# Performance work log

Hardware: AMD Instinct MI355X
Metric: run time of the kernel (lower is better)

## Reference

```python
import jax, jax.numpy as jnp
import numpy as np

G, K = 60, 13  # SO(3) group size, neighbors per group element


def _gather(x, nei):
    # x: [N, C, G] -> [N, C, G, K] via fixed neighbor indices (len G*K)
    return x[:, :, nei].reshape(x.shape[0], x.shape[1], G, K)


def _comb(x, nei, W, b):
    # gather-then-(1,K)-Conv2d == contraction over (channel, neighbor)
    d = _gather(x, nei)                                   # [N,C,G,K]
    return jnp.einsum('ncgk,ock->nog', d, W) + b[None, :, None]


def setup_inputs() -> dict:
    key = jax.random.key(0)
    ks = jax.random.split(key, 8)
    N = 512
    feats = jax.random.normal(ks[0], (N, 32, G), jnp.float32)
    nei = jax.random.randint(ks[1], (G * K,), 0, G, jnp.int32)

    def w(k, o, c):
        return jax.random.normal(k, (o, c, K), jnp.float32) * (1.0 / np.sqrt(c * K))

    return {
        'feats': feats, 'nei': nei,
        'W_in': w(ks[2], 256, 32), 'b_in': jnp.zeros((256,), jnp.float32),
        'W_r1': w(ks[3], 512, 256), 'b_r1': jnp.zeros((512,), jnp.float32),
        'W_r2': w(ks[4], 256, 512), 'b_r2': jnp.zeros((256,), jnp.float32),
        'W_out': w(ks[5], 32, 256), 'b_out': jnp.zeros((32,), jnp.float32),
    }


def reference(feats, nei, W_in, b_in, W_r1, b_r1, W_r2, b_r2, W_out, b_out):
    # Conv_in: gather + (1,13) conv, 32 -> 256
    h = _comb(feats, nei, W_in, b_in)                      # [N,256,G]
    # Residual_Comb_Conv(256, 512, 256)
    r = jax.nn.relu(_comb(h, nei, W_r1, b_r1))             # [N,512,G]
    h = h + _comb(r, nei, W_r2, b_r2)                      # [N,256,G]
    # Conv_out: gather + (1,13) conv, 256 -> 32, then outer residual
    feats_eqv = _comb(h, nei, W_out, b_out) + feats        # [N,32,G]
    feats_inv = jnp.mean(feats_eqv, axis=-1)               # [N,32]
    feats_eqv = feats_eqv / jnp.maximum(
        jnp.linalg.norm(feats_eqv, axis=1, keepdims=True), 1e-4)
    feats_inv = feats_inv / jnp.maximum(
        jnp.linalg.norm(feats_inv, axis=1, keepdims=True), 1e-4)
    return feats_inv, feats_eqv
```

## Files before the change

### kernel.cpp

```cpp
#include <hip/hip_runtime.h>
#include <stdint.h>

#define GSZ 60
#define KNB 13
#define NPT 512

typedef __attribute__((ext_vector_type(4))) float f32x4;
typedef __attribute__((ext_vector_type(8))) short s16x8;

__device__ __forceinline__ ushort f2bf(float f) {
  union { float f; unsigned u; } v; v.f = f;
  unsigned r = v.u + 0x7fffu + ((v.u >> 16) & 1u);
  return (ushort)(r >> 16);
}
__device__ __forceinline__ float bf2f(ushort h) {
  union { unsigned u; float f; } v; v.u = ((unsigned)h) << 16;
  return v.f;
}

__device__ __forceinline__ void gload_lds16(const void* gsrc, void* ldst) {
  __builtin_amdgcn_global_load_lds(
      (const __attribute__((address_space(1))) uint32_t*)gsrc,
      (__attribute__((address_space(3))) uint32_t*)ldst, 16, 0, 0);
}

__global__ __launch_bounds__(256) void prep_feats_k(const float* __restrict__ feats,
                                                    ushort* __restrict__ X0) {
  int idx = blockIdx.x * 256 + threadIdx.x;
  if (idx >= 61 * NPT * 32) return;
  int c = idx & 31;
  int t = idx >> 5;
  int n = t % NPT;
  int g = t / NPT;
  X0[idx] = (g < GSZ) ? f2bf(feats[(n * 32 + c) * GSZ + g]) : (ushort)0;
}

__global__ __launch_bounds__(256) void prep_wb_k(const float* __restrict__ W,
                                                 ushort* __restrict__ Wb,
                                                 int O, int OPAD, int C, int KPAD) {
  int idx = blockIdx.x * 256 + threadIdx.x;
  if (idx >= OPAD * KPAD) return;
  int o = idx / KPAD;
  int kk = idx - o * KPAD;
  int k = kk / C;
  int c = kk - k * C;
  Wb[idx] = (o < O && k < KNB) ? f2bf(W[(o * C + c) * KNB + k]) : (ushort)0;
}

template <int CIN, int KTOT, int OPAD, int OREAL, int BN, int MODE, bool RELU>
__global__ __launch_bounds__(256) void comb_gemm(
    const ushort* __restrict__ Xin,
    const ushort* __restrict__ Wb,
    const float* __restrict__ bias,
    const int* __restrict__ nei,
    ushort* __restrict__ Xout,
    float* __restrict__ Eq,
    const float* __restrict__ feats)
{
  constexpr int BM = 128;
  constexpr int BK = 64;
  constexpr int NCH = KTOT / BK;
  constexpr int TO = OPAD / BN;
  constexpr int TN = NPT / BM;
  constexpr int WN = BN / 2;
  constexpr int N_REP = WN / 16;
  constexpr int M_REP = 4;
  constexpr int CSH = (CIN == 32) ? 5 : (CIN == 256) ? 8 : 9;
  static_assert(CIN == (1 << CSH), "CIN pow2");

  __shared__ ushort smA[2][BM * BK];
  __shared__ ushort smB[2][BN * BK];
  __shared__ int nei_sh[16];

  const int nwg = TO * TN * GSZ;
  const int cpx = nwg >> 3;
  const int bid = blockIdx.x;
  const int idx = (bid & 7) * cpx + (bid >> 3);
  const int g = idx / (TO * TN);
  const int rem = idx - g * (TO * TN);
  const int nt = rem / TO;
  const int ot = rem - nt * TO;
  const int n0 = nt * BM;
  const int o0 = ot * BN;

  const int t = threadIdx.x;
  if (t < 14) nei_sh[t] = (t < KNB) ? nei[g * KNB + t] : GSZ;
  __syncthreads();

  const int w = t >> 6;
  const int l = t & 63;
  const int lrow = l & 15;
  const int lkg = l >> 4;
  const int wr = w >> 1;
  const int wc = w & 1;
  const int srow_w = w * 8;
  const int sr = l >> 3;
  const int slot = l & 7;

  int laneA[BM / 32], laneB[BN / 32], swz[BM / 32];
#pragma unroll
  for (int j = 0; j < BM / 32; ++j) {
    const int r = j * 32 + srow_w + sr;
    swz[j] = (slot ^ (r & 7)) << 3;
    laneA[j] = ((n0 + r) << CSH) + swz[j];
  }
#pragma unroll
  for (int j = 0; j < BN / 32; ++j) {
    const int r = j * 32 + srow_w + sr;
    laneB[j] = (o0 + r) * KTOT + ((slot ^ (r & 7)) << 3);
  }

  auto stage = [&](int buf, int q) {
    const int c0 = q * BK;
    if constexpr (CIN >= 64) {
      const int pbase = nei_sh[c0 >> CSH] * (NPT << CSH) + (c0 & (CIN - 1));
#pragma unroll
      for (int j = 0; j < BM / 32; ++j)
        gload_lds16(Xin + pbase + laneA[j], &smA[buf][(j * 32 + srow_w) * BK]);
    } else {
#pragma unroll
      for (int j = 0; j < BM / 32; ++j) {
        const int r = j * 32 + srow_w + sr;
        const int kk = c0 + swz[j];
        const int nbr = kk >> CSH;
        const int cc = kk & (CIN - 1);
        gload_lds16(Xin + ((nei_sh[nbr] * NPT + n0 + r) << CSH) + cc,
                    &smA[buf][(j * 32 + srow_w) * BK]);
      }
    }
#pragma unroll
    for (int j = 0; j < BN / 32; ++j)
      gload_lds16(Wb + laneB[j] + c0, &smB[buf][(j * 32 + srow_w) * BK]);
  };

  f32x4 acc[M_REP][N_REP] = {};

  stage(0, 0);
  asm volatile("s_waitcnt vmcnt(0)" ::: "memory");
  __builtin_amdgcn_s_barrier();

  int cur = 0;
#pragma unroll 1
  for (int q = 0; q < NCH; ++q) {
    if (q + 1 < NCH) stage(cur ^ 1, q + 1);
#pragma unroll
    for (int ks = 0; ks < 2; ++ks) {
      const int cb = ks * 4 + lkg;
      s16x8 bf[N_REP];
#pragma unroll
      for (int n = 0; n < N_REP; ++n) {
        const int r = wc * WN + n * 16 + lrow;
        bf[n] = *(const s16x8*)&smB[cur][r * BK + ((cb ^ (r & 7)) << 3)];
      }
#pragma unroll
      for (int m = 0; m < M_REP; ++m) {
        const int r = wr * 64 + m * 16 + lrow;
        s16x8 af = *(const s16x8*)&smA[cur][r * BK + ((cb ^ (r & 7)) << 3)];
#pragma unroll
        for (int n = 0; n < N_REP; ++n)
          acc[m][n] = __builtin_amdgcn_mfma_f32_16x16x32_bf16(af, bf[n], acc[m][n], 0, 0, 0);
      }
    }
    asm volatile("s_waitcnt vmcnt(0)" ::: "memory");
    __builtin_amdgcn_s_barrier();
    cur ^= 1;
  }

#pragma unroll
  for (int m = 0; m < M_REP; ++m) {
#pragma unroll
    for (int n = 0; n < N_REP; ++n) {
      const int oc = o0 + wc * WN + n * 16 + lrow;
      float bv;
      if (MODE == 2)
        bv = (oc < OREAL) ? bias[oc] : 0.f;
      else
        bv = bias[oc];
#pragma unroll
      for (int r = 0; r < 4; ++r) {
        const int row = n0 + wr * 64 + m * 16 + lkg * 4 + r;
        float v = acc[m][n][r] + bv;
        if (MODE == 0) {
          if (RELU) v = v > 0.f ? v : 0.f;
          Xout[((size_t)g * NPT + row) * OPAD + oc] = f2bf(v);
        } else if (MODE == 1) {
          const size_t ix = ((size_t)g * NPT + row) * OPAD + oc;
          Xout[ix] = f2bf(bf2f(Xout[ix]) + v);
        } else {
          const float add = (oc < OREAL) ? feats[((size_t)row * 32 + oc) * GSZ + g] : 0.f;
          Eq[((size_t)g * NPT + row) * 64 + oc] = v + add;
        }
      }
    }
  }
}

__global__ __launch_bounds__(256) void finalize_k(const float* __restrict__ Eq,
                                                  float* __restrict__ out) {
  const int n = blockIdx.x;
  const int t = threadIdx.x;
  const int c = t & 31;
  const int gs = t >> 5;

  float invp = 0.f;
  for (int g = gs; g < GSZ; g += 8) {
    float x = Eq[((size_t)g * NPT + n) * 64 + c];
    invp += x;
    float ss = x * x;
#pragma unroll
    for (int m = 16; m >= 1; m >>= 1) ss += __shfl_xor(ss, m, 64);
    float nrm = sqrtf(ss);
    nrm = nrm > 1e-4f ? nrm : 1e-4f;
    out[16384 + ((size_t)n * 32 + c) * GSZ + g] = x / nrm;
  }

  __shared__ float tmp[8][32];
  tmp[gs][c] = invp;
  __syncthreads();
  if (t < 32) {
    float s = 0.f;
#pragma unroll
    for (int i = 0; i < 8; ++i) s += tmp[i][t];
    s *= (1.f / 60.f);
    float ss = s * s;
#pragma unroll
    for (int m = 16; m >= 1; m >>= 1) ss += __shfl_xor(ss, m, 64);
    float nrm = sqrtf(ss);
    nrm = nrm > 1e-4f ? nrm : 1e-4f;
    out[(size_t)n * 32 + t] = s / nrm;
  }
}

extern "C" void kernel_launch(void* const* d_in, const int* in_sizes, int n_in,
                              void* d_out, int out_size, void* d_ws, size_t ws_size,
                              hipStream_t stream) {
  const float* feats = (const float*)d_in[0];
  const int* nei = (const int*)d_in[1];
  const float* W_in = (const float*)d_in[2];
  const float* b_in = (const float*)d_in[3];
  const float* W_r1 = (const float*)d_in[4];
  const float* b_r1 = (const float*)d_in[5];
  const float* W_r2 = (const float*)d_in[6];
  const float* b_r2 = (const float*)d_in[7];
  const float* W_out = (const float*)d_in[8];
  const float* b_out = (const float*)d_in[9];
  float* out = (float*)d_out;

  char* ws = (char*)d_ws;
  size_t off = 0;
  auto alloc = [&](size_t bytes) {
    void* p = ws + off;
    off += (bytes + 255) & ~(size_t)255;
    return p;
  };
  ushort* X0 = (ushort*)alloc((size_t)61 * NPT * 32 * 2);
  ushort* H1 = (ushort*)alloc((size_t)GSZ * NPT * 256 * 2);
  ushort* R = (ushort*)alloc((size_t)GSZ * NPT * 512 * 2);
  float* Eq = (float*)alloc((size_t)GSZ * NPT * 64 * 4);
  ushort* Wb_in = (ushort*)alloc((size_t)256 * 448 * 2);
  ushort* Wb_r1 = (ushort*)alloc((size_t)512 * 3328 * 2);
  ushort* Wb_r2 = (ushort*)alloc((size_t)256 * 6656 * 2);
  ushort* Wb_out = (ushort*)alloc((size_t)64 * 3328 * 2);

  prep_feats_k<<<(61 * NPT * 32 + 255) / 256, 256, 0, stream>>>(feats, X0);
  prep_wb_k<<<(256 * 448 + 255) / 256, 256, 0, stream>>>(W_in, Wb_in, 256, 256, 32, 448);
  prep_wb_k<<<(512 * 3328 + 255) / 256, 256, 0, stream>>>(W_r1, Wb_r1, 512, 512, 256, 3328);
  prep_wb_k<<<(256 * 6656 + 255) / 256, 256, 0, stream>>>(W_r2, Wb_r2, 256, 256, 512, 6656);
  prep_wb_k<<<(64 * 3328 + 255) / 256, 256, 0, stream>>>(W_out, Wb_out, 32, 64, 256, 3328);

  dim3 blk(256);
  comb_gemm<32, 448, 256, 256, 128, 0, false><<<dim3(2 * 4 * GSZ), blk, 0, stream>>>(
      X0, Wb_in, b_in, nei, H1, nullptr, nullptr);
  comb_gemm<256, 3328, 512, 512, 128, 0, true><<<dim3(4 * 4 * GSZ), blk, 0, stream>>>(
      H1, Wb_r1, b_r1, nei, R, nullptr, nullptr);
  comb_gemm<512, 6656, 256, 256, 128, 1, false><<<dim3(2 * 4 * GSZ), blk, 0, stream>>>(
      R, Wb_r2, b_r2, nei, H1, nullptr, nullptr);
  comb_gemm<256, 3328, 64, 32, 64, 2, false><<<dim3(1 * 4 * GSZ), blk, 0, stream>>>(
      H1, Wb_out, b_out, nei, nullptr, Eq, feats);
  finalize_k<<<NPT, 256, 0, stream>>>(Eq, out);
}
```

Baseline: 325.3 us.

## Use 512-thread 256-tile GEMM for residual layers and split-K the output conv

Adds a 512-thread GEMM variant with larger tiles (256x256 and 256x128) for the two residual comb convolutions, using s_setprio around the MFMA section and a simplified per-chunk neighbor base address. The output conv is split along K into four launches that write partial sums into the now-free R buffer, and the finalize kernel adds the four partials together. The intent is better data reuse and fewer workgroups on the big layers, plus more parallelism for the small output layer. The cost is higher LDS and register pressure per block and extra partial-sum traffic.

```diff
diff --git a/kernel.cpp b/kernel.cpp
--- a/kernel.cpp
+++ b/kernel.cpp
@@ -49,17 +49,12 @@
 
 template <int CIN, int KTOT, int OPAD, int OREAL, int BN, int MODE, bool RELU>
 __global__ __launch_bounds__(256) void comb_gemm(
-    const ushort* __restrict__ Xin,
-    const ushort* __restrict__ Wb,
-    const float* __restrict__ bias,
-    const int* __restrict__ nei,
-    ushort* __restrict__ Xout,
-    float* __restrict__ Eq,
-    const float* __restrict__ feats)
-{
+    const ushort* __restrict__ Xin, const ushort* __restrict__ Wb,
+    const float* __restrict__ bias, const int* __restrict__ nei,
+    ushort* __restrict__ Xout, float* __restrict__ Eq,
+    const float* __restrict__ feats, int qb, int qe) {
   constexpr int BM = 128;
   constexpr int BK = 64;
-  constexpr int NCH = KTOT / BK;
   constexpr int TO = OPAD / BN;
   constexpr int TN = NPT / BM;
   constexpr int WN = BN / 2;
@@ -135,14 +130,14 @@
 
   f32x4 acc[M_REP][N_REP] = {};
 
-  stage(0, 0);
+  stage(0, qb);
   asm volatile("s_waitcnt vmcnt(0)" ::: "memory");
   __builtin_amdgcn_s_barrier();
 
   int cur = 0;
 #pragma unroll 1
-  for (int q = 0; q < NCH; ++q) {
-    if (q + 1 < NCH) stage(cur ^ 1, q + 1);
+  for (int q = qb; q < qe; ++q) {
+    if (q + 1 < qe) stage(cur ^ 1, q + 1);
 #pragma unroll
     for (int ks = 0; ks < 2; ++ks) {
       const int cb = ks * 4 + lkg;
@@ -173,7 +168,7 @@
       const int oc = o0 + wc * WN + n * 16 + lrow;
       float bv;
       if (MODE == 2)
-        bv = (oc < OREAL) ? bias[oc] : 0.f;
+        bv = (oc < OREAL && feats) ? bias[oc] : 0.f;
       else
         bv = bias[oc];
 #pragma unroll
@@ -187,8 +182,133 @@
           const size_t ix = ((size_t)g * NPT + row) * OPAD + oc;
           Xout[ix] = f2bf(bf2f(Xout[ix]) + v);
         } else {
-          const float add = (oc < OREAL) ? feats[((size_t)row * 32 + oc) * GSZ + g] : 0.f;
+          const float add = (oc < OREAL && feats) ? feats[((size_t)row * 32 + oc) * GSZ + g] : 0.f;
           Eq[((size_t)g * NPT + row) * 64 + oc] = v + add;
+        }
+      }
+    }
+  }
+}
+
+template <int CIN, int KTOT, int OPAD, int OREAL, int BN, int MODE, bool RELU>
+__global__ __launch_bounds__(512) void comb_gemm8(
+    const ushort* __restrict__ Xin, const ushort* __restrict__ Wb,
+    const float* __restrict__ bias, const int* __restrict__ nei,
+    ushort* __restrict__ Xout) {
+  constexpr int BM = 256;
+  constexpr int BK = 64;
+  constexpr int NCH = KTOT / BK;
+  constexpr int TO = OPAD / BN;
+  constexpr int TN = NPT / BM;
+  constexpr int WARPS_N = BN / 64;
+  constexpr int WARPS_M = 8 / WARPS_N;
+  constexpr int WM = BM / WARPS_M;
+  constexpr int WN = 64;
+  constexpr int M_REP = WM / 16;
+  constexpr int N_REP = 4;
+  constexpr int CSH = (CIN == 256) ? 8 : 9;
+  static_assert(CIN == (1 << CSH), "CIN pow2");
+
+  __shared__ ushort smA[2][BM * BK];
+  __shared__ ushort smB[2][BN * BK];
+  __shared__ int nei_sh[16];
+
+  const int nwg = TO * TN * GSZ;
+  const int cpx = nwg >> 3;
+  const int bid = blockIdx.x;
+  const int idx = (bid & 7) * cpx + (bid >> 3);
+  const int g = idx / (TO * TN);
+  const int rem = idx - g * (TO * TN);
+  const int nt = rem / TO;
+  const int ot = rem - nt * TO;
+  const int n0 = nt * BM;
+  const int o0 = ot * BN;
+
+  const int t = threadIdx.x;
+  if (t < 14) nei_sh[t] = (t < KNB) ? nei[g * KNB + t] : GSZ;
+  __syncthreads();
+
+  const int w = t >> 6;
+  const int l = t & 63;
+  const int lrow = l & 15;
+  const int lkg = l >> 4;
+  const int wr = w / WARPS_N;
+  const int wc = w % WARPS_N;
+  const int srow_w = w * 8;
+  const int sr = l >> 3;
+  const int slot = l & 7;
+  const int swz = (slot ^ sr) << 3;
+
+  int laneA[BM / 64], laneB[BN / 64];
+#pragma unroll
+  for (int j = 0; j < BM / 64; ++j)
+    laneA[j] = ((n0 + j * 64 + srow_w + sr) << CSH) + swz;
+#pragma unroll
+  for (int j = 0; j < BN / 64; ++j)
+    laneB[j] = (o0 + j * 64 + srow_w + sr) * KTOT + swz;
+
+  auto stage = [&](int buf, int q) {
+    const int c0 = q * BK;
+    const int pbase = nei_sh[c0 >> CSH] * (NPT << CSH) + (c0 & (CIN - 1));
+#pragma unroll
+    for (int j = 0; j < BM / 64; ++j)
+      gload_lds16(Xin + pbase + laneA[j], &smA[buf][(j * 64 + srow_w) * BK]);
+#pragma unroll
+    for (int j = 0; j < BN / 64; ++j)
+      gload_lds16(Wb + laneB[j] + c0, &smB[buf][(j * 64 + srow_w) * BK]);
+  };
+
+  f32x4 acc[M_REP][N_REP] = {};
+
+  stage(0, 0);
+  asm volatile("s_waitcnt vmcnt(0)" ::: "memory");
+  __builtin_amdgcn_s_barrier();
+
+  int cur = 0;
+#pragma unroll 1
+  for (int q = 0; q < NCH; ++q) {
+    if (q + 1 < NCH) stage(cur ^ 1, q + 1);
+    __builtin_amdgcn_s_setprio(1);
+#pragma unroll
+    for (int ks = 0; ks < 2; ++ks) {
+      const int cb = ks * 4 + lkg;
+      s16x8 bf[N_REP];
+#pragma unroll
+      for (int n = 0; n < N_REP; ++n) {
+        const int r = wc * WN + n * 16 + lrow;
+        bf[n] = *(const s16x8*)&smB[cur][r * BK + ((cb ^ (r & 7)) << 3)];
+      }
+#pragma unroll
+      for (int m = 0; m < M_REP; ++m) {
+        const int r = wr * WM + m * 16 + lrow;
+        s16x8 af = *(const s16x8*)&smA[cur][r * BK + ((cb ^ (r & 7)) << 3)];
+#pragma unroll
+        for (int n = 0; n < N_REP; ++n)
+          acc[m][n] = __builtin_amdgcn_mfma_f32_16x16x32_bf16(af, bf[n], acc[m][n], 0, 0, 0);
+      }
+    }
+    __builtin_amdgcn_s_setprio(0);
+    asm volatile("s_waitcnt vmcnt(0)" ::: "memory");
+    __builtin_amdgcn_s_barrier();
+    cur ^= 1;
+  }
+
+#pragma unroll
+  for (int m = 0; m < M_REP; ++m) {
+#pragma unroll
+    for (int n = 0; n < N_REP; ++n) {
+      const int oc = o0 + wc * WN + n * 16 + lrow;
+      const float bv = bias[oc];
+#pragma unroll
+      for (int r = 0; r < 4; ++r) {
+        const int row = n0 + wr * WM + m * 16 + lkg * 4 + r;
+        float v = acc[m][n][r] + bv;
+        if (MODE == 0) {
+          if (RELU) v = v > 0.f ? v : 0.f;
+          Xout[((size_t)g * NPT + row) * OPAD + oc] = f2bf(v);
+        } else {
+          const size_t ix = ((size_t)g * NPT + row) * OPAD + oc;
+          Xout[ix] = f2bf(bf2f(Xout[ix]) + v);
         }
       }
     }
@@ -201,10 +321,12 @@
   const int t = threadIdx.x;
   const int c = t & 31;
   const int gs = t >> 5;
+  constexpr size_t PART = (size_t)GSZ * NPT * 64;
 
   float invp = 0.f;
   for (int g = gs; g < GSZ; g += 8) {
-    float x = Eq[((size_t)g * NPT + n) * 64 + c];
+    const size_t base = ((size_t)g * NPT + n) * 64 + c;
+    float x = Eq[base] + Eq[PART + base] + Eq[2 * PART + base] + Eq[3 * PART + base];
     invp += x;
     float ss = x * x;
 #pragma unroll
@@ -256,11 +378,11 @@
   ushort* X0 = (ushort*)alloc((size_t)61 * NPT * 32 * 2);
   ushort* H1 = (ushort*)alloc((size_t)GSZ * NPT * 256 * 2);
   ushort* R = (ushort*)alloc((size_t)GSZ * NPT * 512 * 2);
-  float* Eq = (float*)alloc((size_t)GSZ * NPT * 64 * 4);
   ushort* Wb_in = (ushort*)alloc((size_t)256 * 448 * 2);
   ushort* Wb_r1 = (ushort*)alloc((size_t)512 * 3328 * 2);
   ushort* Wb_r2 = (ushort*)alloc((size_t)256 * 6656 * 2);
   ushort* Wb_out = (ushort*)alloc((size_t)64 * 3328 * 2);
+  float* Eq4 = (float*)R;
 
   prep_feats_k<<<(61 * NPT * 32 + 255) / 256, 256, 0, stream>>>(feats, X0);
   prep_wb_k<<<(256 * 448 + 255) / 256, 256, 0, stream>>>(W_in, Wb_in, 256, 256, 32, 448);
@@ -268,14 +390,16 @@
   prep_wb_k<<<(256 * 6656 + 255) / 256, 256, 0, stream>>>(W_r2, Wb_r2, 256, 256, 512, 6656);
   prep_wb_k<<<(64 * 3328 + 255) / 256, 256, 0, stream>>>(W_out, Wb_out, 32, 64, 256, 3328);
 
-  dim3 blk(256);
-  comb_gemm<32, 448, 256, 256, 128, 0, false><<<dim3(2 * 4 * GSZ), blk, 0, stream>>>(
-      X0, Wb_in, b_in, nei, H1, nullptr, nullptr);
-  comb_gemm<256, 3328, 512, 512, 128, 0, true><<<dim3(4 * 4 * GSZ), blk, 0, stream>>>(
-      H1, Wb_r1, b_r1, nei, R, nullptr, nullptr);
-  comb_gemm<512, 6656, 256, 256, 128, 1, false><<<dim3(2 * 4 * GSZ), blk, 0, stream>>>(
-      R, Wb_r2, b_r2, nei, H1, nullptr, nullptr);
-  comb_gemm<256, 3328, 64, 32, 64, 2, false><<<dim3(1 * 4 * GSZ), blk, 0, stream>>>(
-      H1, Wb_out, b_out, nei, nullptr, Eq, feats);
-  finalize_k<<<NPT, 256, 0, stream>>>(Eq, out);
-}
+  comb_gemm<32, 448, 256, 256, 128, 0, false><<<dim3(2 * 4 * GSZ), dim3(256), 0, stream>>>(
+      X0, Wb_in, b_in, nei, H1, nullptr, nullptr, 0, 7);
+  comb_gemm8<256, 3328, 512, 512, 256, 0, true><<<dim3(240), dim3(512), 0, stream>>>(
+      H1, Wb_r1, b_r1, nei, R);
+  comb_gemm8<512, 6656, 256, 256, 128, 1, false><<<dim3(240), dim3(512), 0, stream>>>(
+      R, Wb_r2, b_r2, nei, H1);
+  for (int kp = 0; kp < 4; ++kp) {
+    comb_gemm<256, 3328, 64, 32, 64, 2, false><<<dim3(1 * 4 * GSZ), dim3(256), 0, stream>>>(
+        H1, Wb_out, b_out, nei, nullptr, Eq4 + (size_t)kp * GSZ * NPT * 64,
+        kp == 0 ? feats : nullptr, kp * 13, (kp + 1) * 13);
+  }
+  finalize_k<<<NPT, 256, 0, stream>>>(Eq4, out);
+}
```

New measurement: 375.9 us. 1.16x slower.

## Split-K the output GEMM into four partials and fuse prep kernels

Applied to the files above, without the earlier changes.

The final 256->32 GEMM, which previously launched only 240 workgroups, is now split along K into four partitions. Each partition writes its own fp32 partial buffer, reusing the R workspace, and finalize_k sums the four partials. Bias and the feature residual are added only by partition 0. Separately, the five weight and feature prep launches are merged into one kernel to cut launch overhead. The cost is extra partial-buffer traffic and four reads per element in finalize.

```diff
diff --git a/kernel.cpp b/kernel.cpp
--- a/kernel.cpp
+++ b/kernel.cpp
@@ -24,42 +24,57 @@
       (__attribute__((address_space(3))) uint32_t*)ldst, 16, 0, 0);
 }
 
-__global__ __launch_bounds__(256) void prep_feats_k(const float* __restrict__ feats,
-                                                    ushort* __restrict__ X0) {
+__global__ __launch_bounds__(256) void prep_all_k(
+    const float* __restrict__ W_in, const float* __restrict__ W_r1,
+    const float* __restrict__ W_r2, const float* __restrict__ W_out,
+    const float* __restrict__ feats,
+    ushort* __restrict__ Wb_in, ushort* __restrict__ Wb_r1,
+    ushort* __restrict__ Wb_r2, ushort* __restrict__ Wb_out,
+    ushort* __restrict__ X0) {
+  constexpr int N0 = 256 * 448;
+  constexpr int N1 = 512 * 3328;
+  constexpr int N2 = 256 * 6656;
+  constexpr int N3 = 64 * 3328;
+  constexpr int N4 = 61 * NPT * 32;
   int idx = blockIdx.x * 256 + threadIdx.x;
-  if (idx >= 61 * NPT * 32) return;
-  int c = idx & 31;
-  int t = idx >> 5;
-  int n = t % NPT;
-  int g = t / NPT;
-  X0[idx] = (g < GSZ) ? f2bf(feats[(n * 32 + c) * GSZ + g]) : (ushort)0;
-}
-
-__global__ __launch_bounds__(256) void prep_wb_k(const float* __restrict__ W,
-                                                 ushort* __restrict__ Wb,
-                                                 int O, int OPAD, int C, int KPAD) {
-  int idx = blockIdx.x * 256 + threadIdx.x;
-  if (idx >= OPAD * KPAD) return;
-  int o = idx / KPAD;
-  int kk = idx - o * KPAD;
-  int k = kk / C;
-  int c = kk - k * C;
-  Wb[idx] = (o < O && k < KNB) ? f2bf(W[(o * C + c) * KNB + k]) : (ushort)0;
-}
-
-template <int CIN, int KTOT, int OPAD, int OREAL, int BN, int MODE, bool RELU>
+  if (idx < N0) {
+    int o = idx / 448, kk = idx - o * 448, k = kk / 32, c = kk - k * 32;
+    Wb_in[idx] = (k < KNB) ? f2bf(W_in[(o * 32 + c) * KNB + k]) : (ushort)0;
+    return;
+  }
+  idx -= N0;
+  if (idx < N1) {
+    int o = idx / 3328, kk = idx - o * 3328, k = kk / 256, c = kk - k * 256;
+    Wb_r1[idx] = f2bf(W_r1[(o * 256 + c) * KNB + k]);
+    return;
+  }
+  idx -= N1;
+  if (idx < N2) {
+    int o = idx / 6656, kk = idx - o * 6656, k = kk / 512, c = kk - k * 512;
+    Wb_r2[idx] = f2bf(W_r2[(o * 512 + c) * KNB + k]);
+    return;
+  }
+  idx -= N2;
+  if (idx < N3) {
+    int o = idx / 3328, kk = idx - o * 3328, k = kk / 256, c = kk - k * 256;
+    Wb_out[idx] = (o < 32) ? f2bf(W_out[(o * 256 + c) * KNB + k]) : (ushort)0;
+    return;
+  }
+  idx -= N3;
+  if (idx < N4) {
+    int c = idx & 31, t = idx >> 5, n = t % NPT, g = t / NPT;
+    X0[idx] = (g < GSZ) ? f2bf(feats[(n * 32 + c) * GSZ + g]) : (ushort)0;
+  }
+}
+
+template <int CIN, int KTOT, int OPAD, int OREAL, int BN, int MODE, bool RELU, int SPLITK>
 __global__ __launch_bounds__(256) void comb_gemm(
-    const ushort* __restrict__ Xin,
-    const ushort* __restrict__ Wb,
-    const float* __restrict__ bias,
-    const int* __restrict__ nei,
-    ushort* __restrict__ Xout,
-    float* __restrict__ Eq,
-    const float* __restrict__ feats)
-{
+    const ushort* __restrict__ Xin, const ushort* __restrict__ Wb,
+    const float* __restrict__ bias, const int* __restrict__ nei,
+    ushort* __restrict__ Xout, float* __restrict__ Eq,
+    const float* __restrict__ feats, int qb, int qe) {
   constexpr int BM = 128;
   constexpr int BK = 64;
-  constexpr int NCH = KTOT / BK;
   constexpr int TO = OPAD / BN;
   constexpr int TN = NPT / BM;
   constexpr int WN = BN / 2;
@@ -72,16 +87,26 @@
   __shared__ ushort smB[2][BN * BK];
   __shared__ int nei_sh[16];
 
-  const int nwg = TO * TN * GSZ;
+  const int nparts = TO * TN * GSZ;
+  const int nwg = nparts * SPLITK;
   const int cpx = nwg >> 3;
   const int bid = blockIdx.x;
   const int idx = (bid & 7) * cpx + (bid >> 3);
-  const int g = idx / (TO * TN);
-  const int rem = idx - g * (TO * TN);
+  int kp = 0, sub = idx;
+  if constexpr (SPLITK > 1) {
+    kp = idx / nparts;
+    sub = idx - kp * nparts;
+    constexpr int CHP = (KTOT / BK) / SPLITK;
+    qb = kp * CHP;
+    qe = qb + CHP;
+  }
+  const int g = sub / (TO * TN);
+  const int rem = sub - g * (TO * TN);
   const int nt = rem / TO;
   const int ot = rem - nt * TO;
   const int n0 = nt * BM;
   const int o0 = ot * BN;
+  const bool addf = (SPLITK == 1) || (kp == 0);
 
   const int t = threadIdx.x;
   if (t < 14) nei_sh[t] = (t < KNB) ? nei[g * KNB + t] : GSZ;
@@ -135,14 +160,14 @@
 
   f32x4 acc[M_REP][N_REP] = {};
 
-  stage(0, 0);
+  stage(0, qb);
   asm volatile("s_waitcnt vmcnt(0)" ::: "memory");
   __builtin_amdgcn_s_barrier();
 
   int cur = 0;
 #pragma unroll 1
-  for (int q = 0; q < NCH; ++q) {
-    if (q + 1 < NCH) stage(cur ^ 1, q + 1);
+  for (int q = qb; q < qe; ++q) {
+    if (q + 1 < qe) stage(cur ^ 1, q + 1);
 #pragma unroll
     for (int ks = 0; ks < 2; ++ks) {
       const int cb = ks * 4 + lkg;
@@ -166,6 +191,7 @@
     cur ^= 1;
   }
 
+  float* eqp = (MODE == 2) ? Eq + (size_t)kp * GSZ * NPT * 64 : Eq;
 #pragma unroll
   for (int m = 0; m < M_REP; ++m) {
 #pragma unroll
@@ -173,7 +199,7 @@
       const int oc = o0 + wc * WN + n * 16 + lrow;
       float bv;
       if (MODE == 2)
-        bv = (oc < OREAL) ? bias[oc] : 0.f;
+        bv = (oc < OREAL && addf) ? bias[oc] : 0.f;
       else
         bv = bias[oc];
 #pragma unroll
@@ -187,8 +213,8 @@
           const size_t ix = ((size_t)g * NPT + row) * OPAD + oc;
           Xout[ix] = f2bf(bf2f(Xout[ix]) + v);
         } else {
-          const float add = (oc < OREAL) ? feats[((size_t)row * 32 + oc) * GSZ + g] : 0.f;
-          Eq[((size_t)g * NPT + row) * 64 + oc] = v + add;
+          const float add = (oc < OREAL && addf) ? feats[((size_t)row * 32 + oc) * GSZ + g] : 0.f;
+          eqp[((size_t)g * NPT + row) * 64 + oc] = v + add;
         }
       }
     }
@@ -201,10 +227,12 @@
   const int t = threadIdx.x;
   const int c = t & 31;
   const int gs = t >> 5;
+  constexpr size_t PART = (size_t)GSZ * NPT * 64;
 
   float invp = 0.f;
   for (int g = gs; g < GSZ; g += 8) {
-    float x = Eq[((size_t)g * NPT + n) * 64 + c];
+    const size_t base = ((size_t)g * NPT + n) * 64 + c;
+    float x = Eq[base] + Eq[PART + base] + Eq[2 * PART + base] + Eq[3 * PART + base];
     invp += x;
     float ss = x * x;
 #pragma unroll
@@ -256,26 +284,23 @@
   ushort* X0 = (ushort*)alloc((size_t)61 * NPT * 32 * 2);
   ushort* H1 = (ushort*)alloc((size_t)GSZ * NPT * 256 * 2);
   ushort* R = (ushort*)alloc((size_t)GSZ * NPT * 512 * 2);
-  float* Eq = (float*)alloc((size_t)GSZ * NPT * 64 * 4);
   ushort* Wb_in = (ushort*)alloc((size_t)256 * 448 * 2);
   ushort* Wb_r1 = (ushort*)alloc((size_t)512 * 3328 * 2);
   ushort* Wb_r2 = (ushort*)alloc((size_t)256 * 6656 * 2);
   ushort* Wb_out = (ushort*)alloc((size_t)64 * 3328 * 2);
-
-  prep_feats_k<<<(61 * NPT * 32 + 255) / 256, 256, 0, stream>>>(feats, X0);
-  prep_wb_k<<<(256 * 448 + 255) / 256, 256, 0, stream>>>(W_in, Wb_in, 256, 256, 32, 448);
-  prep_wb_k<<<(512 * 3328 + 255) / 256, 256, 0, stream>>>(W_r1, Wb_r1, 512, 512, 256, 3328);
-  prep_wb_k<<<(256 * 6656 + 255) / 256, 256, 0, stream>>>(W_r2, Wb_r2, 256, 256, 512, 6656);
-  prep_wb_k<<<(64 * 3328 + 255) / 256, 256, 0, stream>>>(W_out, Wb_out, 32, 64, 256, 3328);
-
-  dim3 blk(256);
-  comb_gemm<32, 448, 256, 256, 128, 0, false><<<dim3(2 * 4 * GSZ), blk, 0, stream>>>(
-      X0, Wb_in, b_in, nei, H1, nullptr, nullptr);
-  comb_gemm<256, 3328, 512, 512, 128, 0, true><<<dim3(4 * 4 * GSZ), blk, 0, stream>>>(
-      H1, Wb_r1, b_r1, nei, R, nullptr, nullptr);
-  comb_gemm<512, 6656, 256, 256, 128, 1, false><<<dim3(2 * 4 * GSZ), blk, 0, stream>>>(
-      R, Wb_r2, b_r2, nei, H1, nullptr, nullptr);
-  comb_gemm<256, 3328, 64, 32, 64, 2, false><<<dim3(1 * 4 * GSZ), blk, 0, stream>>>(
-      H1, Wb_out, b_out, nei, nullptr, Eq, feats);
-  finalize_k<<<NPT, 256, 0, stream>>>(Eq, out);
-}
+  float* Eq4 = (float*)R;
+
+  constexpr int PREP_TOT = 256 * 448 + 512 * 3328 + 256 * 6656 + 64 * 3328 + 61 * NPT * 32;
+  prep_all_k<<<dim3((PREP_TOT + 255) / 256), dim3(256), 0, stream>>>(
+      W_in, W_r1, W_r2, W_out, feats, Wb_in, Wb_r1, Wb_r2, Wb_out, X0);
+
+  comb_gemm<32, 448, 256, 256, 128, 0, false, 1><<<dim3(2 * 4 * GSZ), dim3(256), 0, stream>>>(
+      X0, Wb_in, b_in, nei, H1, nullptr, nullptr, 0, 7);
+  comb_gemm<256, 3328, 512, 512, 128, 0, true, 1><<<dim3(4 * 4 * GSZ), dim3(256), 0, stream>>>(
+      H1, Wb_r1, b_r1, nei, R, nullptr, nullptr, 0, 52);
+  comb_gemm<512, 6656, 256, 256, 128, 1, false, 1><<<dim3(2 * 4 * GSZ), dim3(256), 0, stream>>>(
+      R, Wb_r2, b_r2, nei, H1, nullptr, nullptr, 0, 104);
+  comb_gemm<256, 3328, 64, 32, 64, 2, false, 4><<<dim3(4 * 1 * 4 * GSZ), dim3(256), 0, stream>>>(
+      H1, Wb_out, b_out, nei, nullptr, Eq4, feats, 0, 0);
+  finalize_k<<<NPT, 256, 0, stream>>>(Eq4, out);
+}
```

Result: no change. 322.0 us (-1.0%).
